# Optimization experiments

Hardware: AMD Instinct MI355X
Metric: run time of the kernel (lower is better)

## Reference

```python
import jax, jax.numpy as jnp
import numpy as np

HEIGHT = 8
IN_DIM = 128
OUT_DIM = 8
BATCH = 65536
INT_NODES = 2 ** HEIGHT - 1   # 255
LEAF_NODES = 2 ** HEIGHT      # 256


def _and_weight(height):
    # Fixed +-1 structured routing matrix [leaf, int_nodes] (DGTreg._get_and_layer_params).
    leaf = 2 ** height
    w = np.zeros((leaf, leaf - 1), dtype=np.float32)
    for i in range(height):
        num = 2 ** i
        start = num - 1
        for j in range(start, start + num):
            rb = leaf // num * (j - start)
            rm = rb + leaf // (2 * num)
            re = rb + leaf // num
            w[rb:rm, j] = 1.0
            w[rm:re, j] = -1.0
    return jnp.asarray(w)


def setup_inputs() -> dict:
    key = jax.random.key(0)
    k = jax.random.split(key, 5)
    x = jax.random.normal(k[0], (BATCH, IN_DIM), jnp.float32)
    # orthogonal-ish predicate weight (scaled gaussian), zero bias per module init
    Wp = jax.random.normal(k[1], (INT_NODES, IN_DIM), jnp.float32) / np.sqrt(IN_DIM)
    bp = jnp.zeros((INT_NODES,), jnp.float32)
    Wand = _and_weight(HEIGHT)
    # xavier_uniform for or-layer weights [out_dim, in_dim, leaf]
    lim = np.sqrt(6.0 / (IN_DIM + LEAF_NODES)).astype(np.float32)
    Wor = jax.random.uniform(k[2], (OUT_DIM, IN_DIM, LEAF_NODES), jnp.float32, -lim, lim)
    bor = jax.random.normal(k[3], (OUT_DIM, IN_DIM), jnp.float32) * 0.01
    lim2 = np.sqrt(6.0 / (LEAF_NODES + OUT_DIM)).astype(np.float32)
    action_stds = jax.random.uniform(k[4], (LEAF_NODES, OUT_DIM), jnp.float32, -lim2, lim2)
    return {"x": x, "Wp": Wp, "bp": bp, "Wand": Wand, "Wor": Wor, "bor": bor,
            "action_stds": action_stds}


def reference(x, Wp, bp, Wand, Wor, bor, action_stds):
    sg = jax.lax.stop_gradient
    # predicate layer: [B, int_nodes]
    pred_z = x @ Wp.T + bp
    # ScaleBinarizer1: fac = mean(|z|) per row; binarize to {fac, 0}; straight-through grad
    fac = jnp.mean(jnp.abs(pred_z), axis=-1, keepdims=True)
    binz = jnp.where(pred_z >= 0, fac, 0.0)
    pred_a = pred_z + sg(binz - pred_z)          # forward = binz, grad = identity
    pred_a = 2.0 * pred_a - sg(fac)              # in {+fac, -fac}
    # fixed structured 'and' layer -> softmax over leaves
    and_z = pred_a @ Wand.T                      # [B, leaf]
    and_a = jax.nn.softmax(and_z, axis=-1)
    # Sparser1: keep only max entry per row, straight-through grad
    mx = jnp.max(and_a, axis=-1, keepdims=True)
    sp = jnp.where(and_a >= mx, and_a, 0.0)
    and_a = and_a + sg(sp - and_a)
    # or layers: per-output Linear(leaf->in_dim) then <wt, x>
    wt = jnp.einsum('bl,oil->boi', and_a, Wor) + bor[None]   # [B, out, in]
    out = jnp.einsum('boi,bi->bo', wt, x)                    # [B, out]
    # std head over detached routing weights
    std = jnp.sum(action_stds[None] * sg(and_a)[:, :, None], axis=1)  # [B, out]
    std = jnp.clip(std, -20.0, 2.0)
    return (out, std)
```

## Files before the change

kernel.cpp:

```cpp
#include <hip/hip_runtime.h>

#define BATCH 65536
#define IN_DIM 128
#define INT_NODES 255
#define LEAF 256
#define OUT_DIM 8
#define AMB_TH 4e-3f

typedef float    f4v __attribute__((ext_vector_type(4)));
typedef _Float16 h8v __attribute__((ext_vector_type(8)));

#define LGKM0() __asm__ volatile("s_waitcnt lgkmcnt(0)" ::: "memory")

__global__ __launch_bounds__(256) void prep(const float* __restrict__ Wor,
                                            float* __restrict__ Wor_t,
                                            const float* __restrict__ Wp,
                                            _Float16* __restrict__ Bf) {
    if (blockIdx.x < 64) {
        __shared__ float t[64][65];
        const int rt = blockIdx.x >> 2, ct = blockIdx.x & 3;
        const int r0 = rt * 64, c0 = ct * 64;
        const int tx = threadIdx.x & 63, ty = threadIdx.x >> 6;
#pragma unroll
        for (int p = 0; p < 16; ++p) {
            int r = ty + p * 4;
            t[r][tx] = Wor[(size_t)(r0 + r) * 256 + c0 + tx];
        }
        __syncthreads();
#pragma unroll
        for (int p = 0; p < 16; ++p) {
            int r = ty + p * 4;
            Wor_t[(size_t)(c0 + r) * 1024 + r0 + tx] = t[tx][r];
        }
    } else {
        int slot = (blockIdx.x - 64) * 256 + threadIdx.x;
        int j    = slot & 7;
        int lane = (slot >> 3) & 63;
        int ntg  = (slot >> 9) & 15;
        int ks   = slot >> 13;
        int n = ntg * 16 + (lane & 15);
        int k = ks * 32 + (lane >> 4) * 8 + j;
        float v = (n < INT_NODES) ? Wp[n * IN_DIM + k] : 0.f;
        Bf[slot] = (_Float16)v;
    }
}

__global__ __launch_bounds__(256) void dgt_main(
    const float* __restrict__ x, const float* __restrict__ Wp,
    const float* __restrict__ bp, const _Float16* __restrict__ Bfg,
    const float* __restrict__ Wor_t, const float* __restrict__ bor,
    const float* __restrict__ stds,
    float* __restrict__ out, float* __restrict__ stdo) {

    __shared__ unsigned char sgnS[4][LEAF * 4];
    __shared__ float asumS[4][16 * 16];
    __shared__ float hdS[4][16 * 36];
    __shared__ float psS[4][16];
    __shared__ int   lfS[4][16];

    const int tid  = threadIdx.x;
    const int wave = tid >> 6;
    const int lane = tid & 63;
    const int c = lane & 15;
    const int g = lane >> 4;
    const int rowbase = blockIdx.x * 64 + wave * 16;

    unsigned char* sgn = sgnS[wave];
    float* asum = asumS[wave];
    float* hd = hdS[wave];

    h8v ah[4];
    {
        const float* xb = x + (size_t)(rowbase + c) * IN_DIM;
#pragma unroll
        for (int ks = 0; ks < 4; ++ks) {
            const float* p = xb + ks * 32 + g * 8;
            float4 v0 = *reinterpret_cast<const float4*>(p);
            float4 v1 = *reinterpret_cast<const float4*>(p + 4);
            h8v a;
            a[0] = (_Float16)v0.x; a[1] = (_Float16)v0.y;
            a[2] = (_Float16)v0.z; a[3] = (_Float16)v0.w;
            a[4] = (_Float16)v1.x; a[5] = (_Float16)v1.y;
            a[6] = (_Float16)v1.z; a[7] = (_Float16)v1.w;
            ah[ks] = a;
        }
    }

    const h8v* Bf8 = (const h8v*)Bfg;
    float pp[4] = {0.f, 0.f, 0.f, 0.f};
#pragma unroll
    for (int h = 0; h < 2; ++h) {
        f4v acc[8];
#pragma unroll
        for (int nt = 0; nt < 8; ++nt) acc[nt] = (f4v){0.f, 0.f, 0.f, 0.f};
#pragma unroll
        for (int ks = 0; ks < 4; ++ks)
#pragma unroll
            for (int nt = 0; nt < 8; ++nt) {
                h8v b = Bf8[(ks * 16 + h * 8 + nt) * 64 + lane];
                acc[nt] = __builtin_amdgcn_mfma_f32_16x16x32_f16(ah[ks], b, acc[nt], 0, 0, 0);
            }
#pragma unroll
        for (int nt = 0; nt < 8; ++nt) {
            const int n = h * 128 + nt * 16 + c;
            const float bpv = (n < INT_NODES) ? bp[n] : 0.f;
            unsigned by = 0;
#pragma unroll
            for (int rr = 0; rr < 4; ++rr) {
                float v = acc[nt][rr] + bpv;
                float av = fabsf(v);
                if (n < INT_NODES) pp[rr] += av;
                by |= ((v < 0.f ? 1u : 0u) | (av < AMB_TH ? 2u : 0u)) << (2 * rr);
            }
            sgn[n * 4 + g] = (unsigned char)by;
        }
    }
#pragma unroll
    for (int rr = 0; rr < 4; ++rr) asum[(g * 4 + rr) * 16 + c] = pp[rr];
    LGKM0();

    if (lane < 16) {
        const int r = lane;
        float s = 0.f;
#pragma unroll
        for (int cc = 0; cc < 16; cc += 4) {
            f4v v = *reinterpret_cast<f4v*>(&asum[r * 16 + cc]);
            s += (v[0] + v[1]) + (v[2] + v[3]);
        }
        const float fac = s * (1.0f / (float)INT_NODES);
        const float e = expf(-2.0f * fac);
        const float q = 1.0f + e;
        const float q2 = q * q, q4 = q2 * q2, q8 = q4 * q4;

        int node = 0;
#pragma unroll
        for (int d = 0; d < 8; ++d) {
            unsigned by = sgn[node * 4 + (r >> 2)];
            int code = (int)((by >> ((r & 3) * 2)) & 3u);
            int neg;
            if (code & 2) {
                double zd = (double)bp[node];
                const float* wr = Wp + node * IN_DIM;
                const float* xrow = x + (size_t)(rowbase + r) * IN_DIM;
                for (int k = 0; k < IN_DIM; ++k)
                    zd = fma((double)wr[k], (double)xrow[k], zd);
                neg = (zd < 0.0) ? 1 : 0;
            } else {
                neg = code & 1;
            }
            node = 2 * node + 1 + neg;
        }
        psS[wave][r] = 1.0f / q8;
        lfS[wave][r] = node - INT_NODES;
    }
    LGKM0();

    {
        const int r = lane >> 2, kq = lane & 3;
        const int leaf = lfS[wave][r];
        const float ps = psS[wave][r];
        const float* xr = x + (size_t)(rowbase + r) * IN_DIM;
        const float* wl = Wor_t + (size_t)leaf * 1024;
        float hp[8], tp[8];
#pragma unroll
        for (int o = 0; o < 8; ++o) { hp[o] = 0.f; tp[o] = 0.f; }
#pragma unroll
        for (int step = 0; step < 8; ++step) {
            const int off = (step * 4 + kq) * 4;
            float4 xv = *reinterpret_cast<const float4*>(xr + off);
#pragma unroll
            for (int o = 0; o < 8; ++o) {
                float4 wv = *reinterpret_cast<const float4*>(wl + o * IN_DIM + off);
                float4 bv = *reinterpret_cast<const float4*>(bor + o * IN_DIM + off);
                hp[o] = fmaf(wv.x, xv.x, hp[o]); hp[o] = fmaf(wv.y, xv.y, hp[o]);
                hp[o] = fmaf(wv.z, xv.z, hp[o]); hp[o] = fmaf(wv.w, xv.w, hp[o]);
                tp[o] = fmaf(bv.x, xv.x, tp[o]); tp[o] = fmaf(bv.y, xv.y, tp[o]);
                tp[o] = fmaf(bv.z, xv.z, tp[o]); tp[o] = fmaf(bv.w, xv.w, tp[o]);
            }
        }
#pragma unroll
        for (int o = 0; o < 8; ++o)
            hd[r * 36 + o * 4 + kq] = ps * hp[o] + tp[o];
    }
    LGKM0();

    {
        const int r = lane >> 2, op = lane & 3, o0 = op * 2;
        f4v a = *reinterpret_cast<f4v*>(&hd[r * 36 + o0 * 4]);
        f4v b = *reinterpret_cast<f4v*>(&hd[r * 36 + o0 * 4 + 4]);
        float2 ov;
        ov.x = (a[0] + a[1]) + (a[2] + a[3]);
        ov.y = (b[0] + b[1]) + (b[2] + b[3]);
        const size_t ob = (size_t)(rowbase + r) * OUT_DIM + o0;
        *reinterpret_cast<float2*>(out + ob) = ov;
        const int leaf = lfS[wave][r];
        const float ps = psS[wave][r];
        float2 sv;
        sv.x = fminf(fmaxf(ps * stds[leaf * OUT_DIM + o0],     -20.0f), 2.0f);
        sv.y = fminf(fmaxf(ps * stds[leaf * OUT_DIM + o0 + 1], -20.0f), 2.0f);
        *reinterpret_cast<float2*>(stdo + ob) = sv;
    }
}

extern "C" void kernel_launch(void* const* d_in, const int* in_sizes, int n_in,
                              void* d_out, int out_size, void* d_ws, size_t ws_size,
                              hipStream_t stream) {
    const float* x    = (const float*)d_in[0];
    const float* Wp   = (const float*)d_in[1];
    const float* bp   = (const float*)d_in[2];
    const float* Wor  = (const float*)d_in[4];
    const float* bor  = (const float*)d_in[5];
    const float* stds = (const float*)d_in[6];
    float* out = (float*)d_out;

    char* ws = (char*)d_ws;
    float* wor_t = (float*)(ws);
    _Float16* Bf = (_Float16*)(ws + (1 << 20));

    prep<<<192, 256, 0, stream>>>(Wor, wor_t, Wp, Bf);
    dgt_main<<<BATCH / 64, 256, 0, stream>>>(x, Wp, bp, Bf, wor_t, bor, stds,
                                             out, out + (size_t)BATCH * OUT_DIM);
}
```

Baseline: 122.3 us.

## Use fp16 leaf weights with dot2, MFMA for bias term, vectorize ambiguity fallback

```diff
diff --git a/kernel.cpp b/kernel.cpp
--- a/kernel.cpp
+++ b/kernel.cpp
@@ -9,13 +9,24 @@
 
 typedef float    f4v __attribute__((ext_vector_type(4)));
 typedef _Float16 h8v __attribute__((ext_vector_type(8)));
+typedef _Float16 h2v __attribute__((ext_vector_type(2)));
 
 #define LGKM0() __asm__ volatile("s_waitcnt lgkmcnt(0)" ::: "memory")
 
+__device__ __forceinline__ float fdot2(h2v a, h2v b, float c) {
+#if __has_builtin(__builtin_amdgcn_fdot2)
+    return __builtin_amdgcn_fdot2(a, b, c, false);
+#else
+    return c + (float)a[0] * (float)b[0] + (float)a[1] * (float)b[1];
+#endif
+}
+
 __global__ __launch_bounds__(256) void prep(const float* __restrict__ Wor,
-                                            float* __restrict__ Wor_t,
+                                            _Float16* __restrict__ Wh,
                                             const float* __restrict__ Wp,
-                                            _Float16* __restrict__ Bf) {
+                                            _Float16* __restrict__ Bf,
+                                            const float* __restrict__ bor,
+                                            _Float16* __restrict__ Bb) {
     if (blockIdx.x < 64) {
         __shared__ float t[64][65];
         const int rt = blockIdx.x >> 2, ct = blockIdx.x & 3;
@@ -30,9 +41,9 @@
 #pragma unroll
         for (int p = 0; p < 16; ++p) {
             int r = ty + p * 4;
-            Wor_t[(size_t)(c0 + r) * 1024 + r0 + tx] = t[tx][r];
-        }
-    } else {
+            Wh[(size_t)(c0 + r) * 1024 + r0 + tx] = (_Float16)t[tx][r];
+        }
+    } else if (blockIdx.x < 192) {
         int slot = (blockIdx.x - 64) * 256 + threadIdx.x;
         int j    = slot & 7;
         int lane = (slot >> 3) & 63;
@@ -42,19 +53,29 @@
         int k = ks * 32 + (lane >> 4) * 8 + j;
         float v = (n < INT_NODES) ? Wp[n * IN_DIM + k] : 0.f;
         Bf[slot] = (_Float16)v;
+    } else {
+        int slot = (blockIdx.x - 192) * 256 + threadIdx.x;
+        int j    = slot & 7;
+        int lane = (slot >> 3) & 63;
+        int ks   = slot >> 9;
+        int o = lane & 15;
+        int k = ks * 32 + (lane >> 4) * 8 + j;
+        float v = (o < OUT_DIM) ? bor[o * IN_DIM + k] : 0.f;
+        Bb[slot] = (_Float16)v;
     }
 }
 
 __global__ __launch_bounds__(256) void dgt_main(
     const float* __restrict__ x, const float* __restrict__ Wp,
     const float* __restrict__ bp, const _Float16* __restrict__ Bfg,
-    const float* __restrict__ Wor_t, const float* __restrict__ bor,
+    const _Float16* __restrict__ Bbg, const _Float16* __restrict__ Wh,
     const float* __restrict__ stds,
     float* __restrict__ out, float* __restrict__ stdo) {
 
     __shared__ unsigned char sgnS[4][LEAF * 4];
     __shared__ float asumS[4][16 * 16];
     __shared__ float hdS[4][16 * 36];
+    __shared__ float tbS[4][16 * 8];
     __shared__ float psS[4][16];
     __shared__ int   lfS[4][16];
 
@@ -86,6 +107,19 @@
         }
     }
 
+    {
+        const h8v* Bb8 = (const h8v*)Bbg;
+        f4v tb = (f4v){0.f, 0.f, 0.f, 0.f};
+#pragma unroll
+        for (int ks = 0; ks < 4; ++ks)
+            tb = __builtin_amdgcn_mfma_f32_16x16x32_f16(ah[ks], Bb8[ks * 64 + lane], tb, 0, 0, 0);
+        if (c < OUT_DIM) {
+#pragma unroll
+            for (int rr = 0; rr < 4; ++rr)
+                tbS[wave][(g * 4 + rr) * 8 + c] = tb[rr];
+        }
+    }
+
     const h8v* Bf8 = (const h8v*)Bfg;
     float pp[4] = {0.f, 0.f, 0.f, 0.f};
 #pragma unroll
@@ -117,6 +151,22 @@
     }
 #pragma unroll
     for (int rr = 0; rr < 4; ++rr) asum[(g * 4 + rr) * 16 + c] = pp[rr];
+
+    h2v xh[16];
+    {
+        const float* xr = x + (size_t)(rowbase + (lane >> 2)) * IN_DIM;
+        const int kq = lane & 3;
+#pragma unroll
+        for (int ch = 0; ch < 4; ++ch) {
+            const int base = (ch * 4 + kq) * 8;
+            float4 v0 = *reinterpret_cast<const float4*>(xr + base);
+            float4 v1 = *reinterpret_cast<const float4*>(xr + base + 4);
+            xh[ch * 4 + 0] = (h2v){(_Float16)v0.x, (_Float16)v0.y};
+            xh[ch * 4 + 1] = (h2v){(_Float16)v0.z, (_Float16)v0.w};
+            xh[ch * 4 + 2] = (h2v){(_Float16)v1.x, (_Float16)v1.y};
+            xh[ch * 4 + 3] = (h2v){(_Float16)v1.z, (_Float16)v1.w};
+        }
+    }
     LGKM0();
 
     if (lane < 16) {
@@ -139,11 +189,18 @@
             int code = (int)((by >> ((r & 3) * 2)) & 3u);
             int neg;
             if (code & 2) {
-                double zd = (double)bp[node];
                 const float* wr = Wp + node * IN_DIM;
                 const float* xrow = x + (size_t)(rowbase + r) * IN_DIM;
-                for (int k = 0; k < IN_DIM; ++k)
-                    zd = fma((double)wr[k], (double)xrow[k], zd);
+                double z0 = 0.0, z1 = 0.0, z2 = 0.0, z3 = 0.0;
+                for (int k = 0; k < IN_DIM; k += 4) {
+                    float4 wv = *reinterpret_cast<const float4*>(wr + k);
+                    float4 xv = *reinterpret_cast<const float4*>(xrow + k);
+                    z0 = fma((double)wv.x, (double)xv.x, z0);
+                    z1 = fma((double)wv.y, (double)xv.y, z1);
+                    z2 = fma((double)wv.z, (double)xv.z, z2);
+                    z3 = fma((double)wv.w, (double)xv.w, z3);
+                }
+                double zd = ((z0 + z1) + (z2 + z3)) + (double)bp[node];
                 neg = (zd < 0.0) ? 1 : 0;
             } else {
                 neg = code & 1;
@@ -158,43 +215,43 @@
     {
         const int r = lane >> 2, kq = lane & 3;
         const int leaf = lfS[wave][r];
+        const _Float16* wl = Wh + (size_t)leaf * 1024;
+        float hp[8];
+#pragma unroll
+        for (int o = 0; o < 8; ++o) hp[o] = 0.f;
+#pragma unroll
+        for (int ch = 0; ch < 4; ++ch) {
+            const int base = (ch * 4 + kq) * 8;
+            h2v x0 = xh[ch * 4 + 0], x1 = xh[ch * 4 + 1];
+            h2v x2 = xh[ch * 4 + 2], x3 = xh[ch * 4 + 3];
+#pragma unroll
+            for (int o = 0; o < 8; ++o) {
+                h8v w8 = *reinterpret_cast<const h8v*>(wl + o * IN_DIM + base);
+                h2v w0 = {w8[0], w8[1]}, w1 = {w8[2], w8[3]};
+                h2v w2 = {w8[4], w8[5]}, w3 = {w8[6], w8[7]};
+                hp[o] = fdot2(w0, x0, hp[o]);
+                hp[o] = fdot2(w1, x1, hp[o]);
+                hp[o] = fdot2(w2, x2, hp[o]);
+                hp[o] = fdot2(w3, x3, hp[o]);
+            }
+        }
+#pragma unroll
+        for (int o = 0; o < 8; ++o)
+            hd[r * 36 + o * 4 + kq] = hp[o];
+    }
+    LGKM0();
+
+    {
+        const int r = lane >> 2, op = lane & 3, o0 = op * 2;
         const float ps = psS[wave][r];
-        const float* xr = x + (size_t)(rowbase + r) * IN_DIM;
-        const float* wl = Wor_t + (size_t)leaf * 1024;
-        float hp[8], tp[8];
-#pragma unroll
-        for (int o = 0; o < 8; ++o) { hp[o] = 0.f; tp[o] = 0.f; }
-#pragma unroll
-        for (int step = 0; step < 8; ++step) {
-            const int off = (step * 4 + kq) * 4;
-            float4 xv = *reinterpret_cast<const float4*>(xr + off);
-#pragma unroll
-            for (int o = 0; o < 8; ++o) {
-                float4 wv = *reinterpret_cast<const float4*>(wl + o * IN_DIM + off);
-                float4 bv = *reinterpret_cast<const float4*>(bor + o * IN_DIM + off);
-                hp[o] = fmaf(wv.x, xv.x, hp[o]); hp[o] = fmaf(wv.y, xv.y, hp[o]);
-                hp[o] = fmaf(wv.z, xv.z, hp[o]); hp[o] = fmaf(wv.w, xv.w, hp[o]);
-                tp[o] = fmaf(bv.x, xv.x, tp[o]); tp[o] = fmaf(bv.y, xv.y, tp[o]);
-                tp[o] = fmaf(bv.z, xv.z, tp[o]); tp[o] = fmaf(bv.w, xv.w, tp[o]);
-            }
-        }
-#pragma unroll
-        for (int o = 0; o < 8; ++o)
-            hd[r * 36 + o * 4 + kq] = ps * hp[o] + tp[o];
-    }
-    LGKM0();
-
-    {
-        const int r = lane >> 2, op = lane & 3, o0 = op * 2;
         f4v a = *reinterpret_cast<f4v*>(&hd[r * 36 + o0 * 4]);
         f4v b = *reinterpret_cast<f4v*>(&hd[r * 36 + o0 * 4 + 4]);
         float2 ov;
-        ov.x = (a[0] + a[1]) + (a[2] + a[3]);
-        ov.y = (b[0] + b[1]) + (b[2] + b[3]);
+        ov.x = ps * ((a[0] + a[1]) + (a[2] + a[3])) + tbS[wave][r * 8 + o0];
+        ov.y = ps * ((b[0] + b[1]) + (b[2] + b[3])) + tbS[wave][r * 8 + o0 + 1];
         const size_t ob = (size_t)(rowbase + r) * OUT_DIM + o0;
         *reinterpret_cast<float2*>(out + ob) = ov;
         const int leaf = lfS[wave][r];
-        const float ps = psS[wave][r];
         float2 sv;
         sv.x = fminf(fmaxf(ps * stds[leaf * OUT_DIM + o0],     -20.0f), 2.0f);
         sv.y = fminf(fmaxf(ps * stds[leaf * OUT_DIM + o0 + 1], -20.0f), 2.0f);
@@ -214,10 +271,11 @@
     float* out = (float*)d_out;
 
     char* ws = (char*)d_ws;
-    float* wor_t = (float*)(ws);
-    _Float16* Bf = (_Float16*)(ws + (1 << 20));
-
-    prep<<<192, 256, 0, stream>>>(Wor, wor_t, Wp, Bf);
-    dgt_main<<<BATCH / 64, 256, 0, stream>>>(x, Wp, bp, Bf, wor_t, bor, stds,
+    _Float16* Wh = (_Float16*)(ws);
+    _Float16* Bf = (_Float16*)(ws + (512 << 10));
+    _Float16* Bb = (_Float16*)(ws + (576 << 10));
+
+    prep<<<200, 256, 0, stream>>>(Wor, Wh, Wp, Bf, bor, Bb);
+    dgt_main<<<BATCH / 64, 256, 0, stream>>>(x, Wp, bp, Bf, Bb, Wh, stds,
                                              out, out + (size_t)BATCH * OUT_DIM);
 }
```

After: 113.2 us. 7.4% less time.
